# Performance work log

Measured on AMD Instinct MI355X. Metric: run time of the kernel, lower is better.

## Reference

```python
import jax, jax.numpy as jnp
import numpy as np

HID = 6

def setup_inputs() -> dict:
    key = jax.random.key(0)
    k1, k2, k3, k4 = jax.random.split(key, 4)
    B, IN, OUT = 4194304, 20, 6
    x = jax.random.normal(k1, (B, IN), dtype=jnp.float32)
    # nn.Linear weights: shape [out_features, in_features], bias=False
    W1 = jax.random.normal(k2, (HID, IN), dtype=jnp.float32) / np.sqrt(IN)
    W2 = jax.random.normal(k3, (HID, HID), dtype=jnp.float32) / np.sqrt(HID)
    W5 = jax.random.normal(k4, (OUT, HID), dtype=jnp.float32) / np.sqrt(HID)
    return {"x": x, "W1": W1, "W2": W2, "W5": W5}

def reference(x, W1, W2, W5):
    # x = sigmoid(linear1(x)); x = sigmoid(linear2(x)); x = linear5(x)
    h = jax.nn.sigmoid(x @ W1.T)       # [B, 6]
    h = jax.nn.sigmoid(h @ W2.T)       # [B, 6]
    return h @ W5.T                    # [B, out]
```

## Files before the change

### kernel.cpp

```cpp
#include <hip/hip_runtime.h>

#define NIN  20
#define NHID 6
#define NOUT 6

__device__ __forceinline__ float fsig(float t) {
    return __builtin_amdgcn_rcpf(1.0f + __expf(-t));
}

__global__ __launch_bounds__(256, 4)
void mlp_fused(const float* __restrict__ x,
               const float* __restrict__ W1,
               const float* __restrict__ W2,
               const float* __restrict__ W5,
               float* __restrict__ out,
               long long nrows)
{
    __shared__ float sW1[NHID][NIN];
    __shared__ float sW2[NHID][8];
    __shared__ float sW5[NHID][8];

    const int t = threadIdx.x;
    if (t < 120) sW1[t / 20][t % 20] = W1[t];
    if (t >= 128 && t < 176) {
        int u = t - 128, r = u >> 3, c = u & 7;
        sW2[r][c] = (c < 6) ? W2[r * 6 + c] : 0.0f;
    }
    if (t >= 192 && t < 240) {
        int u = t - 192, r = u >> 3, c = u & 7;
        sW5[r][c] = (c < 6) ? W5[r * 6 + c] : 0.0f;
    }
    __syncthreads();

    const long long row0 = ((long long)blockIdx.x * blockDim.x + t) * 2LL;
    if (row0 + 1 >= nrows + 1) return;

    const float4* __restrict__ xp = (const float4*)(x + row0 * NIN);
    float4 xv[10];
#pragma unroll
    for (int i = 0; i < 10; ++i) xv[i] = xp[i];

    float h0[NHID], h1[NHID];
#pragma unroll
    for (int j = 0; j < NHID; ++j) {
        const float4* wp = (const float4*)(&sW1[j][0]);
        float a0 = 0.0f, a1 = 0.0f;
#pragma unroll
        for (int k = 0; k < 5; ++k) {
            float4 w  = wp[k];
            float4 u0 = xv[k];
            float4 u1 = xv[5 + k];
            a0 = fmaf(u0.x, w.x, a0); a0 = fmaf(u0.y, w.y, a0);
            a0 = fmaf(u0.z, w.z, a0); a0 = fmaf(u0.w, w.w, a0);
            a1 = fmaf(u1.x, w.x, a1); a1 = fmaf(u1.y, w.y, a1);
            a1 = fmaf(u1.z, w.z, a1); a1 = fmaf(u1.w, w.w, a1);
        }
        h0[j] = fsig(a0);
        h1[j] = fsig(a1);
    }

    float g0[NHID], g1[NHID];
#pragma unroll
    for (int j = 0; j < NHID; ++j) {
        float a0 = 0.0f, a1 = 0.0f;
#pragma unroll
        for (int k = 0; k < NHID; ++k) {
            float w = sW2[j][k];
            a0 = fmaf(h0[k], w, a0);
            a1 = fmaf(h1[k], w, a1);
        }
        g0[j] = fsig(a0);
        g1[j] = fsig(a1);
    }

    float o0[NOUT], o1[NOUT];
#pragma unroll
    for (int j = 0; j < NOUT; ++j) {
        float a0 = 0.0f, a1 = 0.0f;
#pragma unroll
        for (int k = 0; k < NHID; ++k) {
            float w = sW5[j][k];
            a0 = fmaf(g0[k], w, a0);
            a1 = fmaf(g1[k], w, a1);
        }
        o0[j] = a0;
        o1[j] = a1;
    }

    float4* __restrict__ op = (float4*)(out + row0 * NOUT);
    op[0] = make_float4(o0[0], o0[1], o0[2], o0[3]);
    op[1] = make_float4(o0[4], o0[5], o1[0], o1[1]);
    op[2] = make_float4(o1[2], o1[3], o1[4], o1[5]);
}

extern "C" void kernel_launch(void* const* d_in, const int* in_sizes, int n_in,
                              void* d_out, int out_size, void* d_ws, size_t ws_size,
                              hipStream_t stream) {
    const float* x  = (const float*)d_in[0];
    const float* W1 = (const float*)d_in[1];
    const float* W2 = (const float*)d_in[2];
    const float* W5 = (const float*)d_in[3];
    float* out = (float*)d_out;

    const long long nrows = (long long)in_sizes[0] / NIN;
    const int block = 256;
    const long long rows_per_block = (long long)block * 2;
    const int grid = (int)((nrows + rows_per_block - 1) / rows_per_block);
    mlp_fused<<<grid, block, 0, stream>>>(x, W1, W2, W5, out, nrows);
}
```

Measured before the change: 463.9 us.

## Stage x rows through padded shared memory for coalesced loads, one row per thread

Each block now loads its 256 rows of x with fully coalesced float4 reads into a padded shared-memory tile, and each thread then reads its row from LDS. Weights are read straight from global memory (scalar/constant cache) rather than staged in shared memory, and each thread handles one row instead of two. This targets the strided per-thread 80-byte vector loads of the old layout, at the cost of an extra LDS round trip, a barrier, twice as many blocks and narrower float2 output stores.

```diff
diff --git a/kernel.cpp b/kernel.cpp
--- a/kernel.cpp
+++ b/kernel.cpp
@@ -3,6 +3,8 @@
 #define NIN  20
 #define NHID 6
 #define NOUT 6
+#define RPB  256
+#define PAD  21
 
 __device__ __forceinline__ float fsig(float t) {
     return __builtin_amdgcn_rcpf(1.0f + __expf(-t));
@@ -14,83 +16,66 @@
                const float* __restrict__ W2,
                const float* __restrict__ W5,
                float* __restrict__ out,
-               long long nrows)
+               int nrows)
 {
-    __shared__ float sW1[NHID][NIN];
-    __shared__ float sW2[NHID][8];
-    __shared__ float sW5[NHID][8];
+    __shared__ float sx[RPB * PAD];
 
     const int t = threadIdx.x;
-    if (t < 120) sW1[t / 20][t % 20] = W1[t];
-    if (t >= 128 && t < 176) {
-        int u = t - 128, r = u >> 3, c = u & 7;
-        sW2[r][c] = (c < 6) ? W2[r * 6 + c] : 0.0f;
-    }
-    if (t >= 192 && t < 240) {
-        int u = t - 192, r = u >> 3, c = u & 7;
-        sW5[r][c] = (c < 6) ? W5[r * 6 + c] : 0.0f;
+    const long long blk_row0 = (long long)blockIdx.x * RPB;
+    const int rows_here = min(RPB, nrows - (int)min((long long)nrows, blk_row0));
+
+    const float4* __restrict__ xp4 = (const float4*)(x + blk_row0 * NIN);
+    const int n4 = rows_here * 5;
+#pragma unroll
+    for (int k = 0; k < 5; ++k) {
+        const int i = t + RPB * k;
+        if (i < n4) {
+            float4 v = xp4[i];
+            const int r = i / 5;
+            const int c = 4 * (i % 5);
+            float* d = &sx[r * PAD + c];
+            d[0] = v.x; d[1] = v.y; d[2] = v.z; d[3] = v.w;
+        }
     }
     __syncthreads();
 
-    const long long row0 = ((long long)blockIdx.x * blockDim.x + t) * 2LL;
-    if (row0 + 1 >= nrows + 1) return;
+    if (t >= rows_here) return;
 
-    const float4* __restrict__ xp = (const float4*)(x + row0 * NIN);
-    float4 xv[10];
+    float xr[NIN];
 #pragma unroll
-    for (int i = 0; i < 10; ++i) xv[i] = xp[i];
+    for (int k = 0; k < NIN; ++k) xr[k] = sx[t * PAD + k];
 
-    float h0[NHID], h1[NHID];
+    float h[NHID];
 #pragma unroll
     for (int j = 0; j < NHID; ++j) {
-        const float4* wp = (const float4*)(&sW1[j][0]);
-        float a0 = 0.0f, a1 = 0.0f;
+        float a = 0.0f;
 #pragma unroll
-        for (int k = 0; k < 5; ++k) {
-            float4 w  = wp[k];
-            float4 u0 = xv[k];
-            float4 u1 = xv[5 + k];
-            a0 = fmaf(u0.x, w.x, a0); a0 = fmaf(u0.y, w.y, a0);
-            a0 = fmaf(u0.z, w.z, a0); a0 = fmaf(u0.w, w.w, a0);
-            a1 = fmaf(u1.x, w.x, a1); a1 = fmaf(u1.y, w.y, a1);
-            a1 = fmaf(u1.z, w.z, a1); a1 = fmaf(u1.w, w.w, a1);
-        }
-        h0[j] = fsig(a0);
-        h1[j] = fsig(a1);
+        for (int k = 0; k < NIN; ++k) a = fmaf(xr[k], W1[j * NIN + k], a);
+        h[j] = fsig(a);
     }
 
-    float g0[NHID], g1[NHID];
+    float g[NHID];
 #pragma unroll
     for (int j = 0; j < NHID; ++j) {
-        float a0 = 0.0f, a1 = 0.0f;
+        float a = 0.0f;
 #pragma unroll
-        for (int k = 0; k < NHID; ++k) {
-            float w = sW2[j][k];
-            a0 = fmaf(h0[k], w, a0);
-            a1 = fmaf(h1[k], w, a1);
-        }
-        g0[j] = fsig(a0);
-        g1[j] = fsig(a1);
+        for (int k = 0; k < NHID; ++k) a = fmaf(h[k], W2[j * NHID + k], a);
+        g[j] = fsig(a);
     }
 
-    float o0[NOUT], o1[NOUT];
+    float o[NOUT];
 #pragma unroll
     for (int j = 0; j < NOUT; ++j) {
-        float a0 = 0.0f, a1 = 0.0f;
+        float a = 0.0f;
 #pragma unroll
-        for (int k = 0; k < NHID; ++k) {
-            float w = sW5[j][k];
-            a0 = fmaf(g0[k], w, a0);
-            a1 = fmaf(g1[k], w, a1);
-        }
-        o0[j] = a0;
-        o1[j] = a1;
+        for (int k = 0; k < NHID; ++k) a = fmaf(g[k], W5[j * NHID + k], a);
+        o[j] = a;
     }
 
-    float4* __restrict__ op = (float4*)(out + row0 * NOUT);
-    op[0] = make_float4(o0[0], o0[1], o0[2], o0[3]);
-    op[1] = make_float4(o0[4], o0[5], o1[0], o1[1]);
-    op[2] = make_float4(o1[2], o1[3], o1[4], o1[5]);
+    float2* __restrict__ op = (float2*)(out + (blk_row0 + t) * NOUT);
+    op[0] = make_float2(o[0], o[1]);
+    op[1] = make_float2(o[2], o[3]);
+    op[2] = make_float2(o[4], o[5]);
 }
 
 extern "C" void kernel_launch(void* const* d_in, const int* in_sizes, int n_in,
@@ -102,9 +87,7 @@
     const float* W5 = (const float*)d_in[3];
     float* out = (float*)d_out;
 
-    const long long nrows = (long long)in_sizes[0] / NIN;
-    const int block = 256;
-    const long long rows_per_block = (long long)block * 2;
-    const int grid = (int)((nrows + rows_per_block - 1) / rows_per_block);
-    mlp_fused<<<grid, block, 0, stream>>>(x, W1, W2, W5, out, nrows);
+    const int nrows = in_sizes[0] / NIN;
+    const int grid  = (nrows + RPB - 1) / RPB;
+    mlp_fused<<<grid, RPB, 0, stream>>>(x, W1, W2, W5, out, nrows);
 }
```

New measurement: 469.4 us. About the same (+1.2%).
